# Kernel optimization log

Hardware: AMD Instinct MI355X
Metric: run time of the kernel (lower is better)

Reference implementation:

```python
import jax, jax.numpy as jnp
import numpy as np

B, S, E, H = 8, 1024, 768, 12
D = E // H  # per-head dim


def setup_inputs() -> dict:
    key = jax.random.key(0)
    ks = jax.random.split(key, 9)
    glorot = lambda k: jax.random.normal(k, (E, E), jnp.float32) * np.sqrt(2.0 / (E + E))
    return {
        "inputs": jax.random.normal(ks[0], (B, S, E), jnp.float32),
        "Wq": glorot(ks[1]), "bq": jnp.zeros((E,), jnp.float32),
        "Wk": glorot(ks[2]), "bk": jnp.zeros((E,), jnp.float32),
        "Wv": glorot(ks[3]), "bv": jnp.zeros((E,), jnp.float32),
        "Wo": glorot(ks[4]), "bo": jnp.zeros((E,), jnp.float32),
    }


def reference(inputs, Wq, bq, Wk, bk, Wv, bv, Wo, bo):
    b, s, e = inputs.shape
    # QKV projections then split heads: [B,S,E] -> [B,H,S,D]
    def heads(x):
        return x.reshape(b, s, H, D).transpose(0, 2, 1, 3)
    q = heads(inputs @ Wq + bq)
    k = heads(inputs @ Wk + bk)
    v = heads(inputs @ Wv + bv)
    scale = 1.0 / jnp.sqrt(jnp.asarray(D, inputs.dtype))
    scores = jnp.einsum("bhqd,bhkd->bhqk", q, k) * scale
    weights = jax.nn.softmax(scores, axis=-1)  # attn_drop rate 0 -> identity
    attn = jnp.einsum("bhqk,bhkd->bhqd", weights, v)
    concat = attn.transpose(0, 2, 1, 3).reshape(b, s, e)
    out = concat @ Wo + bo  # proj_drop rate 0 -> identity
    return out
```

## Files before the change

### kernel.cpp

```cpp
#include <hip/hip_runtime.h>
#include <math.h>

#define BB 8
#define SS 1024
#define EE 768
#define HH 12
#define DD 64
#define MM (BB*SS)

typedef __attribute__((ext_vector_type(8))) short short8;
typedef __attribute__((ext_vector_type(4))) short short4v;
typedef __attribute__((ext_vector_type(4))) float f32x4;
typedef __attribute__((ext_vector_type(4))) int int4v;

static __device__ __forceinline__ short f2bf(float x) {
    unsigned u = __float_as_uint(x);
    u += 0x7fffu + ((u >> 16) & 1u);
    return (short)(u >> 16);
}
static __device__ __forceinline__ short f2bf_fast(float x) {
    return (short)((__float_as_uint(x) + 0x8000u) >> 16);
}

static __device__ __forceinline__ int cvtpk_bf16(float lo, float hi) {
    int r;
    asm("v_cvt_pk_bf16_f32 %0, %1, %2" : "=v"(r) : "v"(lo), "v"(hi));
    return r;
}
static __device__ __forceinline__ short8 i4_to_s8(int4v v) {
    union { int4v i; short8 s; } u; u.i = v; return u.s;
}

static __device__ __forceinline__ void gload_lds16(const void* g, void* l) {
    __builtin_amdgcn_global_load_lds((__attribute__((address_space(1))) void*)g,
                                     (__attribute__((address_space(3))) void*)l,
                                     16, 0, 0);
}

#define BAR __builtin_amdgcn_s_barrier()
#define VMW(n) asm volatile("s_waitcnt vmcnt(" #n ")" ::: "memory")

__global__ __launch_bounds__(256)
void prep(const float* __restrict__ X, short* __restrict__ Xb,
          const float* __restrict__ W0, const float* __restrict__ W1,
          const float* __restrict__ W2, const float* __restrict__ W3,
          short* __restrict__ Wt) {
    const int tid = threadIdx.x;
    if (blockIdx.x < 6144) {
        const long i = ((long)blockIdx.x * 256 + tid) * 4;
        float4 v = *(const float4*)&X[i];
        short4v o;
        o.x = f2bf(v.x); o.y = f2bf(v.y); o.z = f2bf(v.z); o.w = f2bf(v.w);
        *(short4v*)&Xb[i] = o;
        return;
    }
    __shared__ short T[64][72];
    const int id = blockIdx.x - 6144;
    const int z  = id / 144;
    const int r2 = id % 144;
    const int i0 = (r2 / 12) * 64;
    const int j0 = (r2 % 12) * 64;
    const float* sp = (z == 0) ? W0 : (z == 1) ? W1 : (z == 2) ? W2 : W3;
    short* dp = Wt + (long)z * EE * EE;
#pragma unroll
    for (int rep = 0; rep < 4; ++rep) {
        const int r = (tid >> 4) + rep * 16;
        const int c = (tid & 15) * 4;
        float4 v = *(const float4*)&sp[(long)(i0 + r) * EE + j0 + c];
        T[c + 0][r] = f2bf(v.x);
        T[c + 1][r] = f2bf(v.y);
        T[c + 2][r] = f2bf(v.z);
        T[c + 3][r] = f2bf(v.w);
    }
    __syncthreads();
#pragma unroll
    for (int rep = 0; rep < 4; ++rep) {
        const int rr = (tid >> 4) + rep * 16;
        const int cc = (tid & 15) * 4;
        short4v o;
        o.x = T[rr][cc + 0]; o.y = T[rr][cc + 1];
        o.z = T[rr][cc + 2]; o.w = T[rr][cc + 3];
        *(short4v*)&dp[(long)(j0 + rr) * EE + i0 + cc] = o;
    }
}

#define GEMM_CORE(Abase, Bbase, row0, col0)                                     \
    f32x4 acc[4][4];                                                            \
    _Pragma("unroll") for (int i = 0; i < 4; ++i)                               \
        _Pragma("unroll") for (int j = 0; j < 4; ++j)                           \
            acc[i][j] = (f32x4){0.f, 0.f, 0.f, 0.f};                            \
    const int rm = (w & 1) * 64, cn = (w >> 1) * 64;                            \
    for (int k0 = 0; k0 < EE; k0 += 64) {                                       \
        __syncthreads();                                                        \
        _Pragma("unroll") for (int i = 0; i < 4; ++i) {                         \
            const int chunk = w * 256 + i * 64 + lane;                          \
            const int r = chunk >> 3;                                          \
            const int cs = (((chunk & 7) ^ (r & 7)) << 3);                      \
            short* ldsA = Al + (w * 256 + i * 64) * 8;                          \
            short* ldsB = Bl + (w * 256 + i * 64) * 8;                          \
            gload_lds16(&Abase[(long)(row0 + r) * EE + k0 + cs], ldsA);         \
            gload_lds16(&Bbase[(long)(col0 + r) * EE + k0 + cs], ldsB);         \
        }                                                                       \
        __syncthreads();                                                        \
        _Pragma("unroll") for (int ks = 0; ks < 2; ++ks) {                      \
            short8 af[4], bf[4];                                                \
            _Pragma("unroll") for (int t = 0; t < 4; ++t)                       \
                af[t] = *(const short8*)&Al[(rm + t * 16 + m) * 64 +            \
                                            (((ks * 4 + quad) ^ (m & 7)) << 3)]; \
            _Pragma("unroll") for (int t = 0; t < 4; ++t)                       \
                bf[t] = *(const short8*)&Bl[(cn + t * 16 + m) * 64 +            \
                                            (((ks * 4 + quad) ^ (m & 7)) << 3)]; \
            _Pragma("unroll") for (int mt = 0; mt < 4; ++mt)                    \
                _Pragma("unroll") for (int nt = 0; nt < 4; ++nt)                \
                    acc[mt][nt] = __builtin_amdgcn_mfma_f32_16x16x32_bf16(      \
                        af[mt], bf[nt], acc[mt][nt], 0, 0, 0);                  \
        }                                                                       \
    }

#define QSCALE 0.1803368801111204f

#define STG1(Ld, Gbase, gr0, k0)                                              \
    do {                                                                      \
        const int r_ = tid >> 3;                                              \
        const int cs_ = ((tid & 7) ^ (r_ & 7)) << 3;                          \
        gload_lds16(&(Gbase)[(long)((gr0) + r_) * EE + (k0) + cs_],           \
                    (Ld) + w * 512);                                          \
    } while (0)

#define QKV_RDA(Ld, mb)                                                       \
    _Pragma("unroll") for (int t = 0; t < 4; ++t)                             \
        _Pragma("unroll") for (int ks = 0; ks < 2; ++ks)                      \
            af[t][ks] = *(const short8*)&(Ld)[(wr * 128 + ((mb) + t) * 16 + m) * 64 + \
                                              (((ks * 4 + quad) ^ (m & 7)) << 3)];

#define QKV_RDB(Ld)                                                           \
    _Pragma("unroll") for (int t = 0; t < 2; ++t)                             \
        _Pragma("unroll") for (int ks = 0; ks < 2; ++ks)                      \
            bf[t][ks] = *(const short8*)&(Ld)[(wc * 32 + t * 16 + m) * 64 +   \
                                              (((ks * 4 + quad) ^ (m & 7)) << 3)];

#define QKV_MF(mb)                                                            \
    __builtin_amdgcn_s_setprio(1);                                            \
    _Pragma("unroll") for (int mq = 0; mq < 4; ++mq)                          \
        _Pragma("unroll") for (int nq = 0; nq < 2; ++nq)                      \
            _Pragma("unroll") for (int ks = 0; ks < 2; ++ks)                  \
                acc[(mb) + mq][nq] = __builtin_amdgcn_mfma_f32_16x16x32_bf16( \
                    af[mq][ks], bf[nq][ks], acc[(mb) + mq][nq], 0, 0, 0);     \
    __builtin_amdgcn_s_setprio(0);

__global__ __launch_bounds__(512, 2)
void gemm_qkv(const short* __restrict__ Xb, const short* __restrict__ Wt,
              const float* __restrict__ bq, const float* __restrict__ bk,
              const float* __restrict__ bv,
              short* __restrict__ Qb, short* __restrict__ Kb,
              short* __restrict__ Vb) {
    __shared__ short SMEM[49152];
    short* const Ae = SMEM;
    short* const Ao = SMEM + 16384;
    short* const Be = SMEM + 32768;
    short* const Bo = SMEM + 40960;

    const int tid = threadIdx.x;
    const int w = tid >> 6;
    const int m = tid & 15, quad = (tid & 63) >> 4;
    const int wr = w >> 2, wc = w & 3;

    const int flat = blockIdx.x + 18 * blockIdx.y;
    const int id   = (flat & 7) * 72 + (flat >> 3);
    const int lcl  = id % 72;
    const int rt   = (id / 72) * 4 + (lcl & 3);
    const int ct   = lcl >> 2;
    const int row0 = rt * 256;
    const int wsel = ct / 6;
    const int col0w = (ct % 6) * 128;
    const short* Wsel = Wt + (long)wsel * EE * EE;
    const float* bias = (wsel == 0) ? bq : (wsel == 1) ? bk : bv;

    f32x4 acc[8][2];
#pragma unroll
    for (int i = 0; i < 8; ++i)
#pragma unroll
        for (int j = 0; j < 2; ++j) acc[i][j] = (f32x4){0.f, 0.f, 0.f, 0.f};

    STG1(Ae + 0,     Xb,   row0 + 0,    0);
    STG1(Ae + 8192,  Xb,   row0 + 128,  0);
    STG1(Be + 0,     Wsel, col0w + 0,   0);
    STG1(Be + 4096,  Wsel, col0w + 64,  0);
    STG1(Ae + 4096,  Xb,   row0 + 64,   0);
    STG1(Ae + 12288, Xb,   row0 + 192,  0);
    STG1(Bo + 0,     Wsel, col0w + 0,   64);
    STG1(Bo + 4096,  Wsel, col0w + 64,  64);
    STG1(Ao + 0,     Xb,   row0 + 0,    64);
    STG1(Ao + 8192,  Xb,   row0 + 128,  64);
    VMW(6);
    BAR;

#pragma unroll 1
    for (int it = 0; it < 6; ++it) {
        const int kO1 = (2 * it + 1) * 64;
        const int t2 = 2 * it + 2, t3 = 2 * it + 3;
        const int kE2 = (t2 < 12 ? t2 : 11) * 64;
        const int kO3 = (t3 < 12 ? t3 : 11) * 64;
        short8 af[4][2], bf[2][2];
        QKV_RDA(Ae, 0);
        QKV_RDB(Be);
        STG1(Ao + 4096,  Xb, row0 + 64,  kO1);
        STG1(Ao + 12288, Xb, row0 + 192, kO1);
        BAR;
        QKV_MF(0);
        VMW(6);
        BAR;
        QKV_RDA(Ae, 4);
        STG1(Be + 0,     Wsel, col0w + 0,  kE2);
        STG1(Be + 4096,  Wsel, col0w + 64, kE2);
        STG1(Ae + 0,     Xb,   row0 + 0,   kE2);
        STG1(Ae + 8192,  Xb,   row0 + 128, kE2);
        BAR;
        QKV_MF(4);
        VMW(6);
        BAR;
        QKV_RDA(Ao, 0);
        QKV_RDB(Bo);
        STG1(Ae + 4096,  Xb, row0 + 64,  kE2);
        STG1(Ae + 12288, Xb, row0 + 192, kE2);
        BAR;
        QKV_MF(0);
        VMW(6);
        BAR;
        QKV_RDA(Ao, 4);
        STG1(Bo + 0,     Wsel, col0w + 0,  kO3);
        STG1(Bo + 4096,  Wsel, col0w + 64, kO3);
        STG1(Ao + 0,     Xb,   row0 + 0,   kO3);
        STG1(Ao + 8192,  Xb,   row0 + 128, kO3);
        BAR;
        QKV_MF(4);
        VMW(6);
        BAR;
    }

    VMW(0);
    __syncthreads();
    const int b = row0 >> 10, s0 = row0 & 1023;
    short* EP = SMEM;

    if (wsel < 2) {
        const float scale = (wsel == 0) ? QSCALE : 1.0f;
        short* QK = (wsel == 0) ? Qb : Kb;
#pragma unroll
        for (int nt = 0; nt < 2; ++nt) {
            const float bvv = bias[col0w + wc * 32 + nt * 16 + m];
#pragma unroll
            for (int mt = 0; mt < 8; ++mt)
#pragma unroll
                for (int r = 0; r < 4; ++r)
                    EP[(wr * 128 + mt * 16 + quad * 4 + r) * 136 + wc * 32 + nt * 16 + m] =
                        f2bf((acc[mt][nt][r] + bvv) * scale);
        }
        __syncthreads();
#pragma unroll
        for (int rep = 0; rep < 8; ++rep) {
            const int chunk = tid + rep * 512;
            const int row = chunk >> 4;
            const int cc = (chunk & 15) * 8;
            const int colg = col0w + cc;
            const int h = colg >> 6, d = colg & 63;
            short8 v = *(const short8*)&EP[row * 136 + cc];
            *(short8*)&QK[((long)(b * HH + h) * SS + s0 + row) * DD + d] = v;
        }
    } else {
#pragma unroll
        for (int nt = 0; nt < 2; ++nt) {
            const float bvv = bias[col0w + wc * 32 + nt * 16 + m];
#pragma unroll
            for (int mt = 0; mt < 8; ++mt) {
                short4v o;
                o.x = f2bf(acc[mt][nt][0] + bvv);
                o.y = f2bf(acc[mt][nt][1] + bvv);
                o.z = f2bf(acc[mt][nt][2] + bvv);
                o.w = f2bf(acc[mt][nt][3] + bvv);
                *(short4v*)&EP[(wc * 32 + nt * 16 + m) * 264 + wr * 128 + mt * 16 + quad * 4] = o;
            }
        }
        __syncthreads();
#pragma unroll
        for (int rep = 0; rep < 8; ++rep) {
            const int chunk = tid + rep * 512;
            const int col = chunk >> 5;
            const int sc8 = (chunk & 31) * 8;
            const int colg = col0w + col;
            const int h = colg >> 6, d = colg & 63;
            short8 v = *(const short8*)&EP[col * 264 + sc8];
            *(short8*)&Vb[((long)(b * HH + h) * DD + d) * SS + s0 + sc8] = v;
        }
    }
}

__global__ __launch_bounds__(256)
void gemm_proj(const short* __restrict__ Cb, const short* __restrict__ WoT,
               const float* __restrict__ bo, float* __restrict__ out) {
    __shared__ short Al[128 * 64];
    __shared__ short Bl[128 * 64];
    const int tid = threadIdx.x, w = tid >> 6, lane = tid & 63;
    const int m = lane & 15, quad = lane >> 4;

    const int flat = blockIdx.x + 6 * blockIdx.y;
    const int id   = (flat & 7) * 48 + (flat >> 3);
    const int xcd  = id / 48;
    const int lcl  = id % 48;
    const int row0 = (xcd * 8 + (lcl & 7)) * 128;
    const int col0 = (lcl >> 3) * 128;

    GEMM_CORE(Cb, WoT, row0, col0)

#pragma unroll
    for (int nt = 0; nt < 4; ++nt) {
        const int colg = col0 + cn + nt * 16 + m;
        const float bvv = bo[colg];
#pragma unroll
        for (int mt = 0; mt < 4; ++mt)
#pragma unroll
            for (int r = 0; r < 4; ++r) {
                const int srow = row0 + rm + mt * 16 + quad * 4 + r;
                out[(long)srow * EE + colg] = acc[mt][nt][r] + bvv;
            }
    }
}

#define ATTN_STAGE(Kdst, Vdst, k0)                                            \
    do {                                                                      \
        _Pragma("unroll") for (int i = 0; i < 2; ++i) {                       \
            const int chunk = w * 128 + i * 64 + l;                           \
            const int r = chunk >> 3;                                         \
            const int cs = ((chunk & 7) ^ (r & 7)) << 3;                      \
            gload_lds16(&Kg[(long)((k0) + r) * DD + cs],                      \
                        (Kdst) + (w * 128 + i * 64) * 8);                     \
            gload_lds16(&Vg[(long)r * SS + (k0) + cs],                        \
                        (Vdst) + (w * 128 + i * 64) * 8);                     \
        }                                                                     \
    } while (0)

#define ATTN_COMPUTE(Kbuf, Vbuf)                                              \
    do {                                                                      \
        f32x4 sc[2][4];                                                       \
        __builtin_amdgcn_s_setprio(1);                                        \
        _Pragma("unroll") for (int nt = 0; nt < 4; ++nt) {                    \
            const short* kb = (Kbuf) + (nt * 16 + m) * 64;                    \
            short8 a0 = *(const short8*)&kb[(quad ^ (m & 7)) << 3];           \
            short8 a1 = *(const short8*)&kb[((4 + quad) ^ (m & 7)) << 3];     \
            _Pragma("unroll") for (int g = 0; g < 2; ++g) {                   \
                f32x4 a = (f32x4){0.f, 0.f, 0.f, 0.f};                        \
                a = __builtin_amdgcn_mfma_f32_16x16x32_bf16(a0, aq[g][0], a, 0, 0, 0); \
                a = __builtin_amdgcn_mfma_f32_16x16x32_bf16(a1, aq[g][1], a, 0, 0, 0); \
                sc[g][nt] = a;                                                \
            }                                                                 \
        }                                                                     \
        __builtin_amdgcn_s_setprio(0);                                        \
        _Pragma("unroll") for (int g = 0; g < 2; ++g)                         \
            _Pragma("unroll") for (int nt = 0; nt < 4; ++nt)                  \
                _Pragma("unroll") for (int r = 0; r < 4; ++r)                 \
                    sc[g][nt][r] = __builtin_amdgcn_exp2f(sc[g][nt][r]);      \
        short8 ap[2][2];                                                      \
        _Pragma("unroll") for (int g = 0; g < 2; ++g)                         \
            _Pragma("unroll") for (int hf = 0; hf < 2; ++hf) {                \
                int4v wv;                                                     \
                wv.x = cvtpk_bf16(sc[g][2 * hf + 0][0], sc[g][2 * hf + 0][1]); \
                wv.y = cvtpk_bf16(sc[g][2 * hf + 0][2], sc[g][2 * hf + 0][3]); \
                wv.z = cvtpk_bf16(sc[g][2 * hf + 1][0], sc[g][2 * hf + 1][1]); \
                wv.w = cvtpk_bf16(sc[g][2 * hf + 1][2], sc[g][2 * hf + 1][3]); \
                ap[g][hf] = i4_to_s8(wv);                                     \
            }                                                                 \
        __builtin_amdgcn_s_setprio(1);                                        \
        _Pragma("unroll") for (int g = 0; g < 2; ++g) {                       \
            lacc[g] = __builtin_amdgcn_mfma_f32_16x16x32_bf16(ap[g][0], ones, lacc[g], 0, 0, 0); \
            lacc[g] = __builtin_amdgcn_mfma_f32_16x16x32_bf16(ap[g][1], ones, lacc[g], 0, 0, 0); \
        }                                                                     \
        const int rsw = m & 7, hb = (quad & 1) * 4;                           \
        _Pragma("unroll") for (int dt = 0; dt < 4; ++dt) {                    \
            const short* vb = (Vbuf) + (dt * 16 + m) * 64;                    \
            short4v l0 = *(const short4v*)&vb[((((quad >> 1) + 0) ^ rsw) << 3) + hb]; \
            short4v h0 = *(const short4v*)&vb[((((quad >> 1) + 2) ^ rsw) << 3) + hb]; \
            short4v l1 = *(const short4v*)&vb[((((quad >> 1) + 4) ^ rsw) << 3) + hb]; \
            short4v h1 = *(const short4v*)&vb[((((quad >> 1) + 6) ^ rsw) << 3) + hb]; \
            short8 b0 = __builtin_shufflevector(l0, h0, 0, 1, 2, 3, 4, 5, 6, 7); \
            short8 b1 = __builtin_shufflevector(l1, h1, 0, 1, 2, 3, 4, 5, 6, 7); \
            _Pragma("unroll") for (int g = 0; g < 2; ++g) {                   \
                O[g][dt] = __builtin_amdgcn_mfma_f32_16x16x32_bf16(ap[g][0], b0, O[g][dt], 0, 0, 0); \
                O[g][dt] = __builtin_amdgcn_mfma_f32_16x16x32_bf16(ap[g][1], b1, O[g][dt], 0, 0, 0); \
            }                                                                 \
        }                                                                     \
        __builtin_amdgcn_s_setprio(0);                                        \
    } while (0)

__global__ __launch_bounds__(256)
void attn_mfma(const short* __restrict__ Q,
               const short* __restrict__ K,
               const short* __restrict__ Vt,
               short* __restrict__ out) {
    __shared__ short K0l[64 * 64];
    __shared__ short K1l[64 * 64];
    __shared__ short V0l[64 * 64];
    __shared__ short V1l[64 * 64];

    const int tid  = threadIdx.x;
    const int w    = tid >> 6;
    const int l    = tid & 63;
    const int m    = l & 15;
    const int quad = l >> 4;

    const int flat = blockIdx.x + 8 * blockIdx.y + 96 * blockIdx.z;
    const int id   = (flat & 7) * 96 + (flat >> 3);
    const int qt   = id & 7;
    const int bh   = id >> 3;
    const int b    = bh / HH;
    const int h    = bh % HH;
    const int q0   = qt * 128;

    const short* Qg = Q  + (long)bh * SS * DD;
    const short* Kg = K  + (long)bh * SS * DD;
    const short* Vg = Vt + (long)bh * DD * SS;

    short8 aq[2][2];
#pragma unroll
    for (int g = 0; g < 2; ++g) {
        const int row = q0 + w * 32 + g * 16 + m;
        aq[g][0] = *(const short8*)(Qg + (long)row * DD + quad * 8);
        aq[g][1] = *(const short8*)(Qg + (long)row * DD + 32 + quad * 8);
    }

    short8 ones;
#pragma unroll
    for (int i = 0; i < 8; ++i) ones[i] = (short)0x3F80;

    f32x4 O[2][4], lacc[2];
#pragma unroll
    for (int g = 0; g < 2; ++g) {
        lacc[g] = (f32x4){0.f, 0.f, 0.f, 0.f};
#pragma unroll
        for (int dt = 0; dt < 4; ++dt) O[g][dt] = (f32x4){0.f, 0.f, 0.f, 0.f};
    }

    ATTN_STAGE(K0l, V0l, 0);
    __syncthreads();

#pragma unroll 1
    for (int kt2 = 0; kt2 < 8; ++kt2) {
        const int k0 = kt2 * 128;
        ATTN_STAGE(K1l, V1l, k0 + 64);
        ATTN_COMPUTE(K0l, V0l);
        __syncthreads();
        if (kt2 < 7) ATTN_STAGE(K0l, V0l, k0 + 128);
        ATTN_COMPUTE(K1l, V1l);
        __syncthreads();
    }

#pragma unroll
    for (int g = 0; g < 2; ++g)
#pragma unroll
        for (int r = 0; r < 4; ++r) {
            const float inv = 1.0f / lacc[g][r];
            const int qo = q0 + w * 32 + g * 16 + quad * 4 + r;
            short* orow = out + ((long)(b * SS + qo)) * EE + h * DD;
#pragma unroll
            for (int dt = 0; dt < 4; ++dt)
                orow[dt * 16 + m] = f2bf(O[g][dt][r] * inv);
        }
}

extern "C" void kernel_launch(void* const* d_in, const int* in_sizes, int n_in,
                              void* d_out, int out_size, void* d_ws, size_t ws_size,
                              hipStream_t stream) {
    const float* X  = (const float*)d_in[0];
    const float* Wq = (const float*)d_in[1];
    const float* bq = (const float*)d_in[2];
    const float* Wk = (const float*)d_in[3];
    const float* bk = (const float*)d_in[4];
    const float* Wv = (const float*)d_in[5];
    const float* bv = (const float*)d_in[6];
    const float* Wo = (const float*)d_in[7];
    const float* bo = (const float*)d_in[8];

    const long SEG = (long)BB * HH * SS * DD;
    const long WSEG = (long)EE * EE;
    short* Xb = (short*)d_ws;
    short* Wt = Xb + SEG;
    short* Qb = Wt + 4 * WSEG;
    short* Kb = Qb + SEG;
    short* Vb = Kb + SEG;
    short* Cb = Vb + SEG;

    prep<<<dim3(6720), 256, 0, stream>>>(X, Xb, Wq, Wk, Wv, Wo, Wt);

    gemm_qkv<<<dim3(18, 32), 512, 0, stream>>>(Xb, Wt, bq, bk, bv, Qb, Kb, Vb);

    attn_mfma<<<dim3(SS / 128, HH, BB), 256, 0, stream>>>(Qb, Kb, Vb, Cb);

    gemm_proj<<<dim3(6, 64), 256, 0, stream>>>(Cb, Wt + 3 * WSEG, bo,
                                               (float*)d_out);
}
```

Before: 195.9 us.

## Fuse prep, QKV GEMM, attention and projection into one persistent kernel with grid barriers

Replaces the four separate launches with one persistent kernel of 192 blocks. Stages (weight/input conversion, QKV GEMM, attention, output projection) are separated by atomic-counter grid barriers. The goal is to remove launch gaps and inter-kernel idle time. The cost is running every stage on only 192 blocks, which may leave CUs idle and adds barrier spin overhead.

```diff
diff --git a/kernel.cpp b/kernel.cpp
--- a/kernel.cpp
+++ b/kernel.cpp
@@ -7,6 +7,7 @@
 #define HH 12
 #define DD 64
 #define MM (BB*SS)
+#define NBLK 192
 
 typedef __attribute__((ext_vector_type(8))) short short8;
 typedef __attribute__((ext_vector_type(4))) short short4v;
@@ -18,10 +19,6 @@
     u += 0x7fffu + ((u >> 16) & 1u);
     return (short)(u >> 16);
 }
-static __device__ __forceinline__ short f2bf_fast(float x) {
-    return (short)((__float_as_uint(x) + 0x8000u) >> 16);
-}
-
 static __device__ __forceinline__ int cvtpk_bf16(float lo, float hi) {
     int r;
     asm("v_cvt_pk_bf16_f32 %0, %1, %2" : "=v"(r) : "v"(lo), "v"(hi));
@@ -40,82 +37,16 @@
 #define BAR __builtin_amdgcn_s_barrier()
 #define VMW(n) asm volatile("s_waitcnt vmcnt(" #n ")" ::: "memory")
 
-__global__ __launch_bounds__(256)
-void prep(const float* __restrict__ X, short* __restrict__ Xb,
-          const float* __restrict__ W0, const float* __restrict__ W1,
-          const float* __restrict__ W2, const float* __restrict__ W3,
-          short* __restrict__ Wt) {
-    const int tid = threadIdx.x;
-    if (blockIdx.x < 6144) {
-        const long i = ((long)blockIdx.x * 256 + tid) * 4;
-        float4 v = *(const float4*)&X[i];
-        short4v o;
-        o.x = f2bf(v.x); o.y = f2bf(v.y); o.z = f2bf(v.z); o.w = f2bf(v.w);
-        *(short4v*)&Xb[i] = o;
-        return;
-    }
-    __shared__ short T[64][72];
-    const int id = blockIdx.x - 6144;
-    const int z  = id / 144;
-    const int r2 = id % 144;
-    const int i0 = (r2 / 12) * 64;
-    const int j0 = (r2 % 12) * 64;
-    const float* sp = (z == 0) ? W0 : (z == 1) ? W1 : (z == 2) ? W2 : W3;
-    short* dp = Wt + (long)z * EE * EE;
-#pragma unroll
-    for (int rep = 0; rep < 4; ++rep) {
-        const int r = (tid >> 4) + rep * 16;
-        const int c = (tid & 15) * 4;
-        float4 v = *(const float4*)&sp[(long)(i0 + r) * EE + j0 + c];
-        T[c + 0][r] = f2bf(v.x);
-        T[c + 1][r] = f2bf(v.y);
-        T[c + 2][r] = f2bf(v.z);
-        T[c + 3][r] = f2bf(v.w);
+static __device__ __forceinline__ void gridbar(int* cnt, int idx) {
+    __threadfence();
+    __syncthreads();
+    if (threadIdx.x == 0) {
+        __hip_atomic_fetch_add(&cnt[idx], 1, __ATOMIC_ACQ_REL, __HIP_MEMORY_SCOPE_AGENT);
+        while (__hip_atomic_load(&cnt[idx], __ATOMIC_ACQUIRE, __HIP_MEMORY_SCOPE_AGENT) < NBLK)
+            __builtin_amdgcn_s_sleep(2);
     }
     __syncthreads();
-#pragma unroll
-    for (int rep = 0; rep < 4; ++rep) {
-        const int rr = (tid >> 4) + rep * 16;
-        const int cc = (tid & 15) * 4;
-        short4v o;
-        o.x = T[rr][cc + 0]; o.y = T[rr][cc + 1];
-        o.z = T[rr][cc + 2]; o.w = T[rr][cc + 3];
-        *(short4v*)&dp[(long)(j0 + rr) * EE + i0 + cc] = o;
-    }
-}
-
-#define GEMM_CORE(Abase, Bbase, row0, col0)                                     \
-    f32x4 acc[4][4];                                                            \
-    _Pragma("unroll") for (int i = 0; i < 4; ++i)                               \
-        _Pragma("unroll") for (int j = 0; j < 4; ++j)                           \
-            acc[i][j] = (f32x4){0.f, 0.f, 0.f, 0.f};                            \
-    const int rm = (w & 1) * 64, cn = (w >> 1) * 64;                            \
-    for (int k0 = 0; k0 < EE; k0 += 64) {                                       \
-        __syncthreads();                                                        \
-        _Pragma("unroll") for (int i = 0; i < 4; ++i) {                         \
-            const int chunk = w * 256 + i * 64 + lane;                          \
-            const int r = chunk >> 3;                                          \
-            const int cs = (((chunk & 7) ^ (r & 7)) << 3);                      \
-            short* ldsA = Al + (w * 256 + i * 64) * 8;                          \
-            short* ldsB = Bl + (w * 256 + i * 64) * 8;                          \
-            gload_lds16(&Abase[(long)(row0 + r) * EE + k0 + cs], ldsA);         \
-            gload_lds16(&Bbase[(long)(col0 + r) * EE + k0 + cs], ldsB);         \
-        }                                                                       \
-        __syncthreads();                                                        \
-        _Pragma("unroll") for (int ks = 0; ks < 2; ++ks) {                      \
-            short8 af[4], bf[4];                                                \
-            _Pragma("unroll") for (int t = 0; t < 4; ++t)                       \
-                af[t] = *(const short8*)&Al[(rm + t * 16 + m) * 64 +            \
-                                            (((ks * 4 + quad) ^ (m & 7)) << 3)]; \
-            _Pragma("unroll") for (int t = 0; t < 4; ++t)                       \
-                bf[t] = *(const short8*)&Bl[(cn + t * 16 + m) * 64 +            \
-                                            (((ks * 4 + quad) ^ (m & 7)) << 3)]; \
-            _Pragma("unroll") for (int mt = 0; mt < 4; ++mt)                    \
-                _Pragma("unroll") for (int nt = 0; nt < 4; ++nt)                \
-                    acc[mt][nt] = __builtin_amdgcn_mfma_f32_16x16x32_bf16(      \
-                        af[mt], bf[nt], acc[mt][nt], 0, 0, 0);                  \
-        }                                                                       \
-    }
+}
 
 #define QSCALE 0.1803368801111204f
 
@@ -148,195 +79,13 @@
                     af[mq][ks], bf[nq][ks], acc[(mb) + mq][nq], 0, 0, 0);     \
     __builtin_amdgcn_s_setprio(0);
 
-__global__ __launch_bounds__(512, 2)
-void gemm_qkv(const short* __restrict__ Xb, const short* __restrict__ Wt,
-              const float* __restrict__ bq, const float* __restrict__ bk,
-              const float* __restrict__ bv,
-              short* __restrict__ Qb, short* __restrict__ Kb,
-              short* __restrict__ Vb) {
-    __shared__ short SMEM[49152];
-    short* const Ae = SMEM;
-    short* const Ao = SMEM + 16384;
-    short* const Be = SMEM + 32768;
-    short* const Bo = SMEM + 40960;
-
-    const int tid = threadIdx.x;
-    const int w = tid >> 6;
-    const int m = tid & 15, quad = (tid & 63) >> 4;
-    const int wr = w >> 2, wc = w & 3;
-
-    const int flat = blockIdx.x + 18 * blockIdx.y;
-    const int id   = (flat & 7) * 72 + (flat >> 3);
-    const int lcl  = id % 72;
-    const int rt   = (id / 72) * 4 + (lcl & 3);
-    const int ct   = lcl >> 2;
-    const int row0 = rt * 256;
-    const int wsel = ct / 6;
-    const int col0w = (ct % 6) * 128;
-    const short* Wsel = Wt + (long)wsel * EE * EE;
-    const float* bias = (wsel == 0) ? bq : (wsel == 1) ? bk : bv;
-
-    f32x4 acc[8][2];
-#pragma unroll
-    for (int i = 0; i < 8; ++i)
-#pragma unroll
-        for (int j = 0; j < 2; ++j) acc[i][j] = (f32x4){0.f, 0.f, 0.f, 0.f};
-
-    STG1(Ae + 0,     Xb,   row0 + 0,    0);
-    STG1(Ae + 8192,  Xb,   row0 + 128,  0);
-    STG1(Be + 0,     Wsel, col0w + 0,   0);
-    STG1(Be + 4096,  Wsel, col0w + 64,  0);
-    STG1(Ae + 4096,  Xb,   row0 + 64,   0);
-    STG1(Ae + 12288, Xb,   row0 + 192,  0);
-    STG1(Bo + 0,     Wsel, col0w + 0,   64);
-    STG1(Bo + 4096,  Wsel, col0w + 64,  64);
-    STG1(Ao + 0,     Xb,   row0 + 0,    64);
-    STG1(Ao + 8192,  Xb,   row0 + 128,  64);
-    VMW(6);
-    BAR;
-
-#pragma unroll 1
-    for (int it = 0; it < 6; ++it) {
-        const int kO1 = (2 * it + 1) * 64;
-        const int t2 = 2 * it + 2, t3 = 2 * it + 3;
-        const int kE2 = (t2 < 12 ? t2 : 11) * 64;
-        const int kO3 = (t3 < 12 ? t3 : 11) * 64;
-        short8 af[4][2], bf[2][2];
-        QKV_RDA(Ae, 0);
-        QKV_RDB(Be);
-        STG1(Ao + 4096,  Xb, row0 + 64,  kO1);
-        STG1(Ao + 12288, Xb, row0 + 192, kO1);
-        BAR;
-        QKV_MF(0);
-        VMW(6);
-        BAR;
-        QKV_RDA(Ae, 4);
-        STG1(Be + 0,     Wsel, col0w + 0,  kE2);
-        STG1(Be + 4096,  Wsel, col0w + 64, kE2);
-        STG1(Ae + 0,     Xb,   row0 + 0,   kE2);
-        STG1(Ae + 8192,  Xb,   row0 + 128, kE2);
-        BAR;
-        QKV_MF(4);
-        VMW(6);
-        BAR;
-        QKV_RDA(Ao, 0);
-        QKV_RDB(Bo);
-        STG1(Ae + 4096,  Xb, row0 + 64,  kE2);
-        STG1(Ae + 12288, Xb, row0 + 192, kE2);
-        BAR;
-        QKV_MF(0);
-        VMW(6);
-        BAR;
-        QKV_RDA(Ao, 4);
-        STG1(Bo + 0,     Wsel, col0w + 0,  kO3);
-        STG1(Bo + 4096,  Wsel, col0w + 64, kO3);
-        STG1(Ao + 0,     Xb,   row0 + 0,   kO3);
-        STG1(Ao + 8192,  Xb,   row0 + 128, kO3);
-        BAR;
-        QKV_MF(4);
-        VMW(6);
-        BAR;
-    }
-
-    VMW(0);
-    __syncthreads();
-    const int b = row0 >> 10, s0 = row0 & 1023;
-    short* EP = SMEM;
-
-    if (wsel < 2) {
-        const float scale = (wsel == 0) ? QSCALE : 1.0f;
-        short* QK = (wsel == 0) ? Qb : Kb;
-#pragma unroll
-        for (int nt = 0; nt < 2; ++nt) {
-            const float bvv = bias[col0w + wc * 32 + nt * 16 + m];
-#pragma unroll
-            for (int mt = 0; mt < 8; ++mt)
-#pragma unroll
-                for (int r = 0; r < 4; ++r)
-                    EP[(wr * 128 + mt * 16 + quad * 4 + r) * 136 + wc * 32 + nt * 16 + m] =
-                        f2bf((acc[mt][nt][r] + bvv) * scale);
-        }
-        __syncthreads();
-#pragma unroll
-        for (int rep = 0; rep < 8; ++rep) {
-            const int chunk = tid + rep * 512;
-            const int row = chunk >> 4;
-            const int cc = (chunk & 15) * 8;
-            const int colg = col0w + cc;
-            const int h = colg >> 6, d = colg & 63;
-            short8 v = *(const short8*)&EP[row * 136 + cc];
-            *(short8*)&QK[((long)(b * HH + h) * SS + s0 + row) * DD + d] = v;
-        }
-    } else {
-#pragma unroll
-        for (int nt = 0; nt < 2; ++nt) {
-            const float bvv = bias[col0w + wc * 32 + nt * 16 + m];
-#pragma unroll
-            for (int mt = 0; mt < 8; ++mt) {
-                short4v o;
-                o.x = f2bf(acc[mt][nt][0] + bvv);
-                o.y = f2bf(acc[mt][nt][1] + bvv);
-                o.z = f2bf(acc[mt][nt][2] + bvv);
-                o.w = f2bf(acc[mt][nt][3] + bvv);
-                *(short4v*)&EP[(wc * 32 + nt * 16 + m) * 264 + wr * 128 + mt * 16 + quad * 4] = o;
-            }
-        }
-        __syncthreads();
-#pragma unroll
-        for (int rep = 0; rep < 8; ++rep) {
-            const int chunk = tid + rep * 512;
-            const int col = chunk >> 5;
-            const int sc8 = (chunk & 31) * 8;
-            const int colg = col0w + col;
-            const int h = colg >> 6, d = colg & 63;
-            short8 v = *(const short8*)&EP[col * 264 + sc8];
-            *(short8*)&Vb[((long)(b * HH + h) * DD + d) * SS + s0 + sc8] = v;
-        }
-    }
-}
-
-__global__ __launch_bounds__(256)
-void gemm_proj(const short* __restrict__ Cb, const short* __restrict__ WoT,
-               const float* __restrict__ bo, float* __restrict__ out) {
-    __shared__ short Al[128 * 64];
-    __shared__ short Bl[128 * 64];
-    const int tid = threadIdx.x, w = tid >> 6, lane = tid & 63;
-    const int m = lane & 15, quad = lane >> 4;
-
-    const int flat = blockIdx.x + 6 * blockIdx.y;
-    const int id   = (flat & 7) * 48 + (flat >> 3);
-    const int xcd  = id / 48;
-    const int lcl  = id % 48;
-    const int row0 = (xcd * 8 + (lcl & 7)) * 128;
-    const int col0 = (lcl >> 3) * 128;
-
-    GEMM_CORE(Cb, WoT, row0, col0)
-
-#pragma unroll
-    for (int nt = 0; nt < 4; ++nt) {
-        const int colg = col0 + cn + nt * 16 + m;
-        const float bvv = bo[colg];
-#pragma unroll
-        for (int mt = 0; mt < 4; ++mt)
-#pragma unroll
-            for (int r = 0; r < 4; ++r) {
-                const int srow = row0 + rm + mt * 16 + quad * 4 + r;
-                out[(long)srow * EE + colg] = acc[mt][nt][r] + bvv;
-            }
-    }
-}
-
-#define ATTN_STAGE(Kdst, Vdst, k0)                                            \
+#define ATTN_STG8(Kdst, Vdst, k0)                                             \
     do {                                                                      \
-        _Pragma("unroll") for (int i = 0; i < 2; ++i) {                       \
-            const int chunk = w * 128 + i * 64 + l;                           \
-            const int r = chunk >> 3;                                         \
-            const int cs = ((chunk & 7) ^ (r & 7)) << 3;                      \
-            gload_lds16(&Kg[(long)((k0) + r) * DD + cs],                      \
-                        (Kdst) + (w * 128 + i * 64) * 8);                     \
-            gload_lds16(&Vg[(long)r * SS + (k0) + cs],                        \
-                        (Vdst) + (w * 128 + i * 64) * 8);                     \
-        }                                                                     \
+        const int chunk = w * 64 + l;                                         \
+        const int r = chunk >> 3;                                             \
+        const int cs = ((chunk & 7) ^ (r & 7)) << 3;                          \
+        gload_lds16(&Kg[(long)((k0) + r) * DD + cs], (Kdst) + w * 512);       \
+        gload_lds16(&Vg[(long)r * SS + (k0) + cs], (Vdst) + w * 512);         \
     } while (0)
 
 #define ATTN_COMPUTE(Kbuf, Vbuf)                                              \
@@ -391,79 +140,336 @@
         __builtin_amdgcn_s_setprio(0);                                        \
     } while (0)
 
-__global__ __launch_bounds__(256)
-void attn_mfma(const short* __restrict__ Q,
-               const short* __restrict__ K,
-               const short* __restrict__ Vt,
-               short* __restrict__ out) {
-    __shared__ short K0l[64 * 64];
-    __shared__ short K1l[64 * 64];
-    __shared__ short V0l[64 * 64];
-    __shared__ short V1l[64 * 64];
-
-    const int tid  = threadIdx.x;
-    const int w    = tid >> 6;
-    const int l    = tid & 63;
-    const int m    = l & 15;
-    const int quad = l >> 4;
-
-    const int flat = blockIdx.x + 8 * blockIdx.y + 96 * blockIdx.z;
-    const int id   = (flat & 7) * 96 + (flat >> 3);
-    const int qt   = id & 7;
-    const int bh   = id >> 3;
-    const int b    = bh / HH;
-    const int h    = bh % HH;
-    const int q0   = qt * 128;
-
-    const short* Qg = Q  + (long)bh * SS * DD;
-    const short* Kg = K  + (long)bh * SS * DD;
-    const short* Vg = Vt + (long)bh * DD * SS;
-
-    short8 aq[2][2];
-#pragma unroll
-    for (int g = 0; g < 2; ++g) {
-        const int row = q0 + w * 32 + g * 16 + m;
-        aq[g][0] = *(const short8*)(Qg + (long)row * DD + quad * 8);
-        aq[g][1] = *(const short8*)(Qg + (long)row * DD + 32 + quad * 8);
+__global__ __launch_bounds__(512)
+void fused(const float* __restrict__ X,
+           const float* __restrict__ W0, const float* __restrict__ W1,
+           const float* __restrict__ W2, const float* __restrict__ W3,
+           const float* __restrict__ bq, const float* __restrict__ bk,
+           const float* __restrict__ bv, const float* __restrict__ bo,
+           short* __restrict__ Xb, short* __restrict__ Wt,
+           short* __restrict__ Qb, short* __restrict__ Kb,
+           short* __restrict__ Vb, short* __restrict__ Cb,
+           float* __restrict__ out, int* bar) {
+    __shared__ short SMEM[49152];
+    const int tid = threadIdx.x;
+    const int w = tid >> 6;
+    const int l = tid & 63;
+    const int m = tid & 15, quad = (tid & 63) >> 4;
+    const int xcd = blockIdx.x & 7;
+    const int slot = blockIdx.x >> 3;
+
+    {
+        short (*T)[72] = (short(*)[72])SMEM;
+#pragma unroll 1
+        for (int t = 0; t < 3; ++t) {
+            const int wid = blockIdx.x * 3 + t;
+            const int z = wid / 144, r2 = wid % 144;
+            const int i0 = (r2 / 12) * 64, j0 = (r2 % 12) * 64;
+            const float* sp = (z == 0) ? W0 : (z == 1) ? W1 : (z == 2) ? W2 : W3;
+            short* dp = Wt + (long)z * EE * EE;
+#pragma unroll
+            for (int rep = 0; rep < 2; ++rep) {
+                const int r = (tid >> 4) + rep * 32;
+                const int c = (tid & 15) * 4;
+                float4 v = *(const float4*)&sp[(long)(i0 + r) * EE + j0 + c];
+                T[c + 0][r] = f2bf(v.x);
+                T[c + 1][r] = f2bf(v.y);
+                T[c + 2][r] = f2bf(v.z);
+                T[c + 3][r] = f2bf(v.w);
+            }
+            __syncthreads();
+#pragma unroll
+            for (int rep = 0; rep < 2; ++rep) {
+                const int rr = (tid >> 4) + rep * 32;
+                const int cc = (tid & 15) * 4;
+                short4v o;
+                o.x = T[rr][cc + 0]; o.y = T[rr][cc + 1];
+                o.z = T[rr][cc + 2]; o.w = T[rr][cc + 3];
+                *(short4v*)&dp[(long)(j0 + rr) * EE + i0 + cc] = o;
+            }
+            __syncthreads();
+        }
+        const long base = (long)blockIdx.x * 512 + tid;
+#pragma unroll 4
+        for (int it2 = 0; it2 < 16; ++it2) {
+            const long q = (base + (long)it2 * (NBLK * 512)) * 4;
+            float4 v = *(const float4*)&X[q];
+            short4v o;
+            o.x = f2bf(v.x); o.y = f2bf(v.y); o.z = f2bf(v.z); o.w = f2bf(v.w);
+            *(short4v*)&Xb[q] = o;
+        }
     }
-
-    short8 ones;
-#pragma unroll
-    for (int i = 0; i < 8; ++i) ones[i] = (short)0x3F80;
-
-    f32x4 O[2][4], lacc[2];
-#pragma unroll
-    for (int g = 0; g < 2; ++g) {
-        lacc[g] = (f32x4){0.f, 0.f, 0.f, 0.f};
-#pragma unroll
-        for (int dt = 0; dt < 4; ++dt) O[g][dt] = (f32x4){0.f, 0.f, 0.f, 0.f};
+    gridbar(bar, 0);
+
+    {
+        short* const Ae = SMEM;
+        short* const Ao = SMEM + 16384;
+        short* const Be = SMEM + 32768;
+        short* const Bo = SMEM + 40960;
+        const int wr = w >> 2, wc = w & 3;
+#pragma unroll 1
+        for (int rnd = 0; rnd < 3; ++rnd) {
+            const int id = xcd * 72 + rnd * 24 + slot;
+            const int lcl = id % 72;
+            const int rt = xcd * 4 + (lcl & 3);
+            const int ct = lcl >> 2;
+            const int row0 = rt * 256;
+            const int wsel = ct / 6;
+            const int col0w = (ct % 6) * 128;
+            const short* Wsel = Wt + (long)wsel * EE * EE;
+            const float* bias = (wsel == 0) ? bq : (wsel == 1) ? bk : bv;
+
+            f32x4 acc[8][2];
+#pragma unroll
+            for (int i = 0; i < 8; ++i)
+#pragma unroll
+                for (int j = 0; j < 2; ++j) acc[i][j] = (f32x4){0.f, 0.f, 0.f, 0.f};
+
+            STG1(Ae + 0,     Xb,   row0 + 0,    0);
+            STG1(Ae + 8192,  Xb,   row0 + 128,  0);
+            STG1(Be + 0,     Wsel, col0w + 0,   0);
+            STG1(Be + 4096,  Wsel, col0w + 64,  0);
+            STG1(Ae + 4096,  Xb,   row0 + 64,   0);
+            STG1(Ae + 12288, Xb,   row0 + 192,  0);
+            STG1(Bo + 0,     Wsel, col0w + 0,   64);
+            STG1(Bo + 4096,  Wsel, col0w + 64,  64);
+            STG1(Ao + 0,     Xb,   row0 + 0,    64);
+            STG1(Ao + 8192,  Xb,   row0 + 128,  64);
+            VMW(6);
+            BAR;
+
+#pragma unroll 1
+            for (int it = 0; it < 6; ++it) {
+                const int kO1 = (2 * it + 1) * 64;
+                const int t2 = 2 * it + 2, t3 = 2 * it + 3;
+                const int kE2 = (t2 < 12 ? t2 : 11) * 64;
+                const int kO3 = (t3 < 12 ? t3 : 11) * 64;
+                short8 af[4][2], bf[2][2];
+                QKV_RDA(Ae, 0);
+                QKV_RDB(Be);
+                STG1(Ao + 4096,  Xb, row0 + 64,  kO1);
+                STG1(Ao + 12288, Xb, row0 + 192, kO1);
+                BAR;
+                QKV_MF(0);
+                VMW(6);
+                BAR;
+                QKV_RDA(Ae, 4);
+                STG1(Be + 0,     Wsel, col0w + 0,  kE2);
+                STG1(Be + 4096,  Wsel, col0w + 64, kE2);
+                STG1(Ae + 0,     Xb,   row0 + 0,   kE2);
+                STG1(Ae + 8192,  Xb,   row0 + 128, kE2);
+                BAR;
+                QKV_MF(4);
+                VMW(6);
+                BAR;
+                QKV_RDA(Ao, 0);
+                QKV_RDB(Bo);
+                STG1(Ae + 4096,  Xb, row0 + 64,  kE2);
+                STG1(Ae + 12288, Xb, row0 + 192, kE2);
+                BAR;
+                QKV_MF(0);
+                VMW(6);
+                BAR;
+                QKV_RDA(Ao, 4);
+                STG1(Bo + 0,     Wsel, col0w + 0,  kO3);
+                STG1(Bo + 4096,  Wsel, col0w + 64, kO3);
+                STG1(Ao + 0,     Xb,   row0 + 0,   kO3);
+                STG1(Ao + 8192,  Xb,   row0 + 128, kO3);
+                BAR;
+                QKV_MF(4);
+                VMW(6);
+                BAR;
+            }
+
+            VMW(0);
+            __syncthreads();
+            const int b = row0 >> 10, s0 = row0 & 1023;
+            short* EP = SMEM;
+            if (wsel < 2) {
+                const float scale = (wsel == 0) ? QSCALE : 1.0f;
+                short* QK = (wsel == 0) ? Qb : Kb;
+#pragma unroll
+                for (int nt = 0; nt < 2; ++nt) {
+                    const float bvv = bias[col0w + wc * 32 + nt * 16 + m];
+#pragma unroll
+                    for (int mt = 0; mt < 8; ++mt)
+#pragma unroll
+                        for (int r = 0; r < 4; ++r)
+                            EP[(wr * 128 + mt * 16 + quad * 4 + r) * 136 + wc * 32 + nt * 16 + m] =
+                                f2bf((acc[mt][nt][r] + bvv) * scale);
+                }
+                __syncthreads();
+#pragma unroll
+                for (int rep = 0; rep < 8; ++rep) {
+                    const int chunk = tid + rep * 512;
+                    const int row = chunk >> 4;
+                    const int cc = (chunk & 15) * 8;
+                    const int colg = col0w + cc;
+                    const int h = colg >> 6, d = colg & 63;
+                    short8 v = *(const short8*)&EP[row * 136 + cc];
+                    *(short8*)&QK[((long)(b * HH + h) * SS + s0 + row) * DD + d] = v;
+                }
+            } else {
+#pragma unroll
+                for (int nt = 0; nt < 2; ++nt) {
+                    const float bvv = bias[col0w + wc * 32 + nt * 16 + m];
+#pragma unroll
+                    for (int mt = 0; mt < 8; ++mt) {
+                        short4v o;
+                        o.x = f2bf(acc[mt][nt][0] + bvv);
+                        o.y = f2bf(acc[mt][nt][1] + bvv);
+                        o.z = f2bf(acc[mt][nt][2] + bvv);
+                        o.w = f2bf(acc[mt][nt][3] + bvv);
+                        *(short4v*)&EP[(wc * 32 + nt * 16 + m) * 264 + wr * 128 + mt * 16 + quad * 4] = o;
+                    }
+                }
+                __syncthreads();
+#pragma unroll
+                for (int rep = 0; rep < 8; ++rep) {
+                    const int chunk = tid + rep * 512;
+                    const int col = chunk >> 5;
+                    const int sc8 = (chunk & 31) * 8;
+                    const int colg = col0w + col;
+                    const int h = colg >> 6, d = colg & 63;
+                    short8 v = *(const short8*)&EP[col * 264 + sc8];
+                    *(short8*)&Vb[((long)(b * HH + h) * DD + d) * SS + s0 + sc8] = v;
+                }
+            }
+            __syncthreads();
+        }
     }
-
-    ATTN_STAGE(K0l, V0l, 0);
-    __syncthreads();
-
+    gridbar(bar, 1);
+
+    {
+        short* const K0l = SMEM;
+        short* const K1l = SMEM + 4096;
+        short* const V0l = SMEM + 8192;
+        short* const V1l = SMEM + 12288;
 #pragma unroll 1
-    for (int kt2 = 0; kt2 < 8; ++kt2) {
-        const int k0 = kt2 * 128;
-        ATTN_STAGE(K1l, V1l, k0 + 64);
-        ATTN_COMPUTE(K0l, V0l);
-        __syncthreads();
-        if (kt2 < 7) ATTN_STAGE(K0l, V0l, k0 + 128);
-        ATTN_COMPUTE(K1l, V1l);
-        __syncthreads();
+        for (int rnd = 0; rnd < 2; ++rnd) {
+            const int vid = xcd * 48 + rnd * 24 + slot;
+            const int bh = vid >> 2, st = vid & 3;
+            const int b = bh / HH, h = bh % HH;
+            const int q0 = st * 256;
+
+            const short* Qg = Qb + (long)bh * SS * DD;
+            const short* Kg = Kb + (long)bh * SS * DD;
+            const short* Vg = Vb + (long)bh * DD * SS;
+
+            short8 aq[2][2];
+#pragma unroll
+            for (int g = 0; g < 2; ++g) {
+                const int row = q0 + w * 32 + g * 16 + m;
+                aq[g][0] = *(const short8*)(Qg + (long)row * DD + quad * 8);
+                aq[g][1] = *(const short8*)(Qg + (long)row * DD + 32 + quad * 8);
+            }
+            short8 ones;
+#pragma unroll
+            for (int i = 0; i < 8; ++i) ones[i] = (short)0x3F80;
+
+            f32x4 O[2][4], lacc[2];
+#pragma unroll
+            for (int g = 0; g < 2; ++g) {
+                lacc[g] = (f32x4){0.f, 0.f, 0.f, 0.f};
+#pragma unroll
+                for (int dt = 0; dt < 4; ++dt) O[g][dt] = (f32x4){0.f, 0.f, 0.f, 0.f};
+            }
+
+            ATTN_STG8(K0l, V0l, 0);
+            __syncthreads();
+#pragma unroll 1
+            for (int kt2 = 0; kt2 < 8; ++kt2) {
+                const int k0 = kt2 * 128;
+                ATTN_STG8(K1l, V1l, k0 + 64);
+                ATTN_COMPUTE(K0l, V0l);
+                __syncthreads();
+                if (kt2 < 7) ATTN_STG8(K0l, V0l, k0 + 128);
+                ATTN_COMPUTE(K1l, V1l);
+                __syncthreads();
+            }
+#pragma unroll
+            for (int g = 0; g < 2; ++g)
+#pragma unroll
+                for (int r = 0; r < 4; ++r) {
+                    const float inv = 1.0f / lacc[g][r];
+                    const int qo = q0 + w * 32 + g * 16 + quad * 4 + r;
+                    short* orow = Cb + ((long)(b * SS + qo)) * EE + h * DD;
+#pragma unroll
+                    for (int dt = 0; dt < 4; ++dt)
+                        orow[dt * 16 + m] = f2bf(O[g][dt][r] * inv);
+                }
+        }
     }
-
-#pragma unroll
-    for (int g = 0; g < 2; ++g)
-#pragma unroll
-        for (int r = 0; r < 4; ++r) {
-            const float inv = 1.0f / lacc[g][r];
-            const int qo = q0 + w * 32 + g * 16 + quad * 4 + r;
-            short* orow = out + ((long)(b * SS + qo)) * EE + h * DD;
-#pragma unroll
-            for (int dt = 0; dt < 4; ++dt)
-                orow[dt * 16 + m] = f2bf(O[g][dt][r] * inv);
+    gridbar(bar, 2);
+
+    {
+        short* const Al = SMEM;
+        short* const Bl = SMEM + 8192;
+        const short* WoT = Wt + (long)3 * EE * EE;
+        const int rt = xcd * 8 + (slot & 7);
+        const int ct = slot >> 3;
+        const int row0 = rt * 128;
+        const int col0 = ct * 256;
+        const int rm2 = (w >> 2) * 64, cn2 = (w & 3) * 64;
+
+        f32x4 acc[4][4];
+#pragma unroll
+        for (int i = 0; i < 4; ++i)
+#pragma unroll
+            for (int j = 0; j < 4; ++j) acc[i][j] = (f32x4){0.f, 0.f, 0.f, 0.f};
+
+#pragma unroll 1
+        for (int k0 = 0; k0 < EE; k0 += 64) {
+            __syncthreads();
+#pragma unroll
+            for (int j = 0; j < 2; ++j) {
+                const int c = tid + j * 512;
+                const int r = c >> 3;
+                const int cs = ((c & 7) ^ (r & 7)) << 3;
+                gload_lds16(&Cb[(long)(row0 + r) * EE + k0 + cs],
+                            Al + (j * 512 + w * 64) * 8);
+            }
+#pragma unroll
+            for (int j = 0; j < 4; ++j) {
+                const int c = tid + j * 512;
+                const int r = c >> 3;
+                const int cs = ((c & 7) ^ (r & 7)) << 3;
+                gload_lds16(&WoT[(long)(col0 + r) * EE + k0 + cs],
+                            Bl + (j * 512 + w * 64) * 8);
+            }
+            __syncthreads();
+#pragma unroll
+            for (int ks = 0; ks < 2; ++ks) {
+                short8 af[4], bf[4];
+#pragma unroll
+                for (int t = 0; t < 4; ++t)
+                    af[t] = *(const short8*)&Al[(rm2 + t * 16 + m) * 64 +
+                                                (((ks * 4 + quad) ^ (m & 7)) << 3)];
+#pragma unroll
+                for (int t = 0; t < 4; ++t)
+                    bf[t] = *(const short8*)&Bl[(cn2 + t * 16 + m) * 64 +
+                                                (((ks * 4 + quad) ^ (m & 7)) << 3)];
+#pragma unroll
+                for (int mt = 0; mt < 4; ++mt)
+#pragma unroll
+                    for (int nt = 0; nt < 4; ++nt)
+                        acc[mt][nt] = __builtin_amdgcn_mfma_f32_16x16x32_bf16(
+                            af[mt], bf[nt], acc[mt][nt], 0, 0, 0);
+            }
         }
+#pragma unroll
+        for (int nt = 0; nt < 4; ++nt) {
+            const int colg = col0 + cn2 + nt * 16 + m;
+            const float bvv = bo[colg];
+#pragma unroll
+            for (int mt = 0; mt < 4; ++mt)
+#pragma unroll
+                for (int r = 0; r < 4; ++r) {
+                    const int srow = row0 + rm2 + mt * 16 + quad * 4 + r;
+                    out[(long)srow * EE + colg] = acc[mt][nt][r] + bvv;
+                }
+        }
+    }
 }
 
 extern "C" void kernel_launch(void* const* d_in, const int* in_sizes, int n_in,
@@ -487,13 +493,10 @@
     short* Kb = Qb + SEG;
     short* Vb = Kb + SEG;
     short* Cb = Vb + SEG;
-
-    prep<<<dim3(6720), 256, 0, stream>>>(X, Xb, Wq, Wk, Wv, Wo, Wt);
-
-    gemm_qkv<<<dim3(18, 32), 512, 0, stream>>>(Xb, Wt, bq, bk, bv, Qb, Kb, Vb);
-
-    attn_mfma<<<dim3(SS / 128, HH, BB), 256, 0, stream>>>(Qb, Kb, Vb, Cb);
-
-    gemm_proj<<<dim3(6, 64), 256, 0, stream>>>(Cb, Wt + 3 * WSEG, bo,
-                                               (float*)d_out);
-}
+    int*   bar = (int*)(Cb + SEG);
+
+    hipMemsetAsync(bar, 0, 64, stream);
+    fused<<<dim3(NBLK), 512, 0, stream>>>(X, Wq, Wk, Wv, Wo, bq, bk, bv, bo,
+                                          Xb, Wt, Qb, Kb, Vb, Cb,
+                                          (float*)d_out, bar);
+}
```

After: 351.4 us. 79.4% more time.
